# Optimization experiments

Measured on AMD Instinct MI355X. Metric: run time of the kernel, lower is better.

Reference implementation:

```python
import jax, jax.numpy as jnp
import numpy as np

N_USERS = 100000
N_ITEMS = 50000
N_NODES = N_USERS + N_ITEMS
DIM = 64
N_HOPS = 3
NNZ = 3200000
BATCH = 4096
K = 4
DECAY = 1e-4


def setup_inputs() -> dict:
    key = jax.random.key(0)
    ks = jax.random.split(key, 8)
    user_embed = jax.random.normal(ks[0], (N_USERS, DIM), dtype=jnp.float32) * 0.1
    item_embed = jax.random.normal(ks[1], (N_ITEMS, DIM), dtype=jnp.float32) * 0.1
    adj_rows = jax.random.randint(ks[2], (NNZ,), 0, N_NODES, dtype=jnp.int32)
    adj_cols = jax.random.randint(ks[3], (NNZ,), 0, N_NODES, dtype=jnp.int32)
    # normalized-adjacency-like small positive values
    adj_vals = jax.random.uniform(ks[4], (NNZ,), dtype=jnp.float32) * 0.05
    users = jax.random.randint(ks[5], (BATCH,), 0, N_USERS, dtype=jnp.int32)
    pos_items = jax.random.randint(ks[6], (BATCH,), 0, N_ITEMS, dtype=jnp.int32)
    neg_items = jax.random.randint(ks[7], (BATCH, K), 0, N_ITEMS, dtype=jnp.int32)
    return {"user_embed": user_embed, "item_embed": item_embed,
            "adj_vals": adj_vals, "adj_rows": adj_rows, "adj_cols": adj_cols,
            "users": users, "pos_items": pos_items, "neg_items": neg_items}


def _gcn(user_embed, item_embed, adj_vals, adj_rows, adj_cols):
    """LightGCN propagation: n_hops of SpMM, stack per-hop embeddings."""
    all_embed = jnp.concatenate([user_embed, item_embed], axis=0)  # [N, d]
    agg = all_embed
    embs = [all_embed]
    for _ in range(N_HOPS):
        msg = adj_vals[:, None] * agg[adj_cols]                    # [nnz, d]
        agg = jax.ops.segment_sum(msg, adj_rows, num_segments=N_NODES)
        embs.append(agg)
    embs = jnp.stack(embs, axis=1)                                 # [N, hops+1, d]
    return embs[:N_USERS], embs[N_USERS:]


def reference(user_embed, item_embed, adj_vals, adj_rows, adj_cols,
              users, pos_items, neg_items):
    user_gcn, item_gcn = _gcn(user_embed, item_embed, adj_vals, adj_rows, adj_cols)
    u_g = user_gcn[users]            # [B, hops+1, d]
    p_g = item_gcn[pos_items]        # [B, hops+1, d]
    n_g = item_gcn[neg_items]        # [B, K, hops+1, d]
    # pooling == 'mean' over hop axis
    u_e = u_g.mean(axis=1)
    pos_e = p_g.mean(axis=1)
    neg_e = n_g.mean(axis=2)         # [B, K, d]
    pos_scores = jnp.sum(u_e * pos_e, axis=-1)                     # [B]
    neg_scores = jnp.sum(u_e[:, None, :] * neg_e, axis=-1)         # [B, K]
    # BCE with logits: labels 1 for pos, 0 for neg
    pos_loss = jax.nn.softplus(-pos_scores)
    neg_loss = jax.nn.softplus(neg_scores).sum(axis=1)
    mf_loss = pos_loss + neg_loss
    regularize = (jnp.sum(u_g[:, 0, :] ** 2)
                  + jnp.sum(p_g[:, 0, :] ** 2)
                  + jnp.sum(n_g[:, :, 0, :] ** 2)) / 2.0
    emb_loss = DECAY * regularize / BATCH
    return mf_loss.mean() + emb_loss
```

## Files before the change

### kernel.cpp

```cpp
#include <hip/hip_runtime.h>
#include <hip/hip_bf16.h>
#include <math.h>

#define N_USERS 100000
#define N_ITEMS 50000
#define N_NODES 150000
#define DIM     64
#define N_HOPS  3
#define NNZ     3200000
#define BATCH   4096
#define KNEG    4
#define DECAY   1e-4f
#define BATCH_TOT (BATCH * (2 + KNEG))

#define NBUCK   586
#define NCHUNK  1024
#define CHUNK   (NNZ / NCHUNK)
#define CAP     8192
#define BH_N    (NBUCK * NCHUNK)
#define S1_N    ((BH_N + 255) / 256)
#define S2_N    ((S1_N + 255) / 256)

typedef unsigned short ushort_t;
typedef unsigned int uint_t;
typedef unsigned long long u64_t;
typedef float v2f __attribute__((ext_vector_type(2)));

#if __has_builtin(__builtin_amdgcn_cvt_pk_f32_fp8) && __has_builtin(__builtin_amdgcn_cvt_pk_fp8_f32)
#define HAVE_FP8_CVT 1
#else
#define HAVE_FP8_CVT 0
#endif

#if !HAVE_FP8_CVT
__device__ __forceinline__ float dec1_(uint_t b) {
    uint_t s = b >> 7, e = (b >> 3) & 15, m = b & 7;
    float mag = e ? __uint_as_float(((e + 120u) << 23) | (m << 20))
                  : (float)m * 0.001953125f;
    return s ? -mag : mag;
}
__device__ __forceinline__ uint_t enc1_(float x) {
    float ax = fabsf(x);
    uint_t s = (__float_as_uint(x) >> 31) << 7;
    if (!(ax > 0.f)) return s;
    if (ax >= 448.f) return s | 0x7E;
    if (ax < 0.015625f) {
        int m = (int)rintf(ax * 512.0f);
        if (m >= 8) return s | 0x08;
        return s | (uint_t)m;
    }
    uint_t u = __float_as_uint(ax);
    u += 0x7FFFF + ((u >> 20) & 1);
    int e = (int)((u >> 23) & 0xFF) - 127 + 7;
    if (e >= 16) return s | 0x7E;
    if (e <= 0)  return s | 0x08;
    return s | ((uint_t)e << 3) | ((u >> 20) & 7);
}
#endif

__device__ __forceinline__ void dec4(uint_t u, float* f) {
#if HAVE_FP8_CVT
    v2f lo = __builtin_amdgcn_cvt_pk_f32_fp8(u, false);
    v2f hi = __builtin_amdgcn_cvt_pk_f32_fp8(u, true);
    f[0] = lo[0]; f[1] = lo[1]; f[2] = hi[0]; f[3] = hi[1];
#else
    f[0] = dec1_(u & 255); f[1] = dec1_((u >> 8) & 255);
    f[2] = dec1_((u >> 16) & 255); f[3] = dec1_(u >> 24);
#endif
}

__device__ __forceinline__ uint_t enc4(const float* f) {
#if HAVE_FP8_CVT
    int t = __builtin_amdgcn_cvt_pk_fp8_f32(f[0], f[1], 0, false);
    t = __builtin_amdgcn_cvt_pk_fp8_f32(f[2], f[3], t, true);
    return (uint_t)t;
#else
    return enc1_(f[0]) | (enc1_(f[1]) << 8) | (enc1_(f[2]) << 16) | (enc1_(f[3]) << 24);
#endif
}


__global__ void k_bhist(const int* __restrict__ rows, int* __restrict__ bh) {
    __shared__ int hist[NBUCK];
    int t = threadIdx.x, b = blockIdx.x;
    for (int i = t; i < NBUCK; i += 256) hist[i] = 0;
    __syncthreads();
    int base = b * CHUNK;
    for (int e = base + t; e < base + CHUNK; e += 256)
        atomicAdd(&hist[rows[e] >> 8], 1);
    __syncthreads();
    for (int i = t; i < NBUCK; i += 256)
        bh[(size_t)i * NCHUNK + b] = hist[i];
}

__global__ void k_scanA(int* __restrict__ data, int* __restrict__ bsums, int n) {
    __shared__ int lds[256];
    int t = threadIdx.x;
    int i = blockIdx.x * 256 + t;
    int v = (i < n) ? data[i] : 0;
    lds[t] = v; __syncthreads();
    for (int o = 1; o < 256; o <<= 1) {
        int x = (t >= o) ? lds[t - o] : 0;
        __syncthreads();
        lds[t] += x;
        __syncthreads();
    }
    if (i < n) data[i] = lds[t] - v;
    if (t == 255) bsums[blockIdx.x] = lds[t];
}

__global__ void k_scan_small(int* __restrict__ data, int n) {
    __shared__ int lds[1024];
    int t = threadIdx.x;
    int v = (t < n) ? data[t] : 0;
    lds[t] = v; __syncthreads();
    for (int o = 1; o < 1024; o <<= 1) {
        int x = (t >= o) ? lds[t - o] : 0;
        __syncthreads();
        lds[t] += x;
        __syncthreads();
    }
    if (t < n) data[t] = lds[t] - v;
}

__global__ void k_addback(int* __restrict__ data, const int* __restrict__ offs, int n) {
    int i = blockIdx.x * blockDim.x + threadIdx.x;
    if (i < n) data[i] += offs[i >> 8];
}

__global__ void k_scatter(const int* __restrict__ rows, const int* __restrict__ cols,
                          const float* __restrict__ vals, const int* __restrict__ bh,
                          u64_t* __restrict__ ebuf) {
    __shared__ int offs[NBUCK];
    int t = threadIdx.x, b = blockIdx.x;
    for (int i = t; i < NBUCK; i += 256)
        offs[i] = bh[(size_t)i * NCHUNK + b];
    __syncthreads();
    int base = b * CHUNK;
    for (int e = base + t; e < base + CHUNK; e += 256) {
        int r = rows[e];
        int slot = atomicAdd(&offs[r >> 8], 1);
        u64_t pk = ((u64_t)(uint_t)__float_as_int(vals[e]) << 32)
                 | ((u64_t)(r & 255) << 18) | (u64_t)cols[e];
        ebuf[slot] = pk;
    }
}

__global__ void k_bucket_csr(const u64_t* __restrict__ ebuf, const int* __restrict__ bh,
                             int2* __restrict__ edges, int* __restrict__ row_ptr) {
    __shared__ u64_t stage[CAP];
    __shared__ int hist[256];
    __shared__ int sbuf[256];
    int t = threadIdx.x, b = blockIdx.x;
    int S = bh[(size_t)b * NCHUNK];
    int E = (b + 1 < NBUCK) ? bh[(size_t)(b + 1) * NCHUNK] : NNZ;
    int cnt = E - S;
    if (cnt > CAP) cnt = CAP;
    hist[t] = 0;
    __syncthreads();
    for (int i = t; i < cnt; i += 256) {
        u64_t v = ebuf[S + i];
        stage[i] = v;
        atomicAdd(&hist[(int)((v >> 18) & 255)], 1);
    }
    __syncthreads();
    int v = hist[t];
    sbuf[t] = v; __syncthreads();
    for (int o = 1; o < 256; o <<= 1) {
        int x = (t >= o) ? sbuf[t - o] : 0;
        __syncthreads();
        sbuf[t] += x;
        __syncthreads();
    }
    int excl = sbuf[t] - v;
    int grow = (b << 8) + t;
    if (grow < N_NODES) row_ptr[grow] = S + excl;
    if (b == 0 && t == 0) row_ptr[N_NODES] = NNZ;
    hist[t] = excl;
    __syncthreads();
    for (int i = t; i < cnt; i += 256) {
        u64_t pk = stage[i];
        int rl = (int)((pk >> 18) & 255);
        int slot = atomicAdd(&hist[rl], 1);
        edges[S + slot] = make_int2((int)(pk & 0x3FFFF), (int)(pk >> 32));
    }
}


__global__ void k_tofp8(const float* __restrict__ ue, const float* __restrict__ ie,
                        uint2* __restrict__ outq) {
    int idx = blockIdx.x * blockDim.x + threadIdx.x;
    const int total8 = N_NODES * DIM / 8;
    if (idx >= total8) return;
    const int u8 = N_USERS * DIM / 8;
    const float4* src = (idx < u8) ? (const float4*)ue + 2 * (size_t)idx
                                   : (const float4*)ie + 2 * (size_t)(idx - u8);
    float4 a = src[0], b = src[1];
    float fa[4] = {a.x, a.y, a.z, a.w};
    float fb[4] = {b.x, b.y, b.z, b.w};
    outq[idx] = make_uint2(enc4(fa), enc4(fb));
}

__device__ __forceinline__ void fma8(uint2 r, float v, float* acc) {
    float f[4];
    dec4(r.x, f);
    acc[0] += v * f[0]; acc[1] += v * f[1]; acc[2] += v * f[2]; acc[3] += v * f[3];
    dec4(r.y, f);
    acc[4] += v * f[0]; acc[5] += v * f[1]; acc[6] += v * f[2]; acc[7] += v * f[3];
}

__device__ __forceinline__ void row_accum8(const uint2* __restrict__ srcq,
                                           const int2* __restrict__ edges,
                                           int s, int e, int oct, int ol,
                                           float* acc) {
    int i = s;
    for (; i + 16 <= e; i += 16) {
        int2 e0 = edges[i + oct];
        int2 e1 = edges[i + 8 + oct];
        uint2 r0 = srcq[(size_t)e0.x * 8 + ol];
        uint2 r1 = srcq[(size_t)e1.x * 8 + ol];
        fma8(r0, __int_as_float(e0.y), acc);
        fma8(r1, __int_as_float(e1.y), acc);
    }
    for (; i + 8 <= e; i += 8) {
        int2 ed = edges[i + oct];
        uint2 r = srcq[(size_t)ed.x * 8 + ol];
        fma8(r, __int_as_float(ed.y), acc);
    }
    int rem = e - i;
    if (oct < rem) {
        int2 ed = edges[i + oct];
        uint2 r = srcq[(size_t)ed.x * 8 + ol];
        fma8(r, __int_as_float(ed.y), acc);
    }
}

__device__ __forceinline__ void oct_reduce(float* acc) {
    #pragma unroll
    for (int j = 0; j < 8; ++j) {
        acc[j] += __shfl_xor(acc[j], 8);
        acc[j] += __shfl_xor(acc[j], 16);
        acc[j] += __shfl_xor(acc[j], 32);
    }
}

__global__ void k_spmm(const uint2* __restrict__ srcq, uint2* __restrict__ outq,
                       const int* __restrict__ row_ptr, const int2* __restrict__ edges) {
    int w = (blockIdx.x * blockDim.x + threadIdx.x) >> 6;
    int lane = threadIdx.x & 63;
    if (w >= N_NODES) return;
    int oct = lane >> 3, ol = lane & 7;
    int s = row_ptr[w], e = row_ptr[w + 1];
    float acc[8] = {0.f, 0.f, 0.f, 0.f, 0.f, 0.f, 0.f, 0.f};
    row_accum8(srcq, edges, s, e, oct, ol, acc);
    oct_reduce(acc);
    if (oct == 0)
        outq[(size_t)w * 8 + ol] = make_uint2(enc4(acc), enc4(acc + 4));
}

__device__ __forceinline__ void batch_map(int w, const int* __restrict__ users,
                                          const int* __restrict__ pos, const int* __restrict__ neg,
                                          float* u_acc, float* p_acc, float* n_acc,
                                          int& node, float*& dst) {
    if (w < BATCH)            { node = users[w];                        dst = u_acc + (size_t)w * DIM; }
    else if (w < 2 * BATCH)   { int j = w - BATCH;     node = N_USERS + pos[j]; dst = p_acc + (size_t)j * DIM; }
    else                      { int j = w - 2 * BATCH; node = N_USERS + neg[j]; dst = n_acc + (size_t)j * DIM; }
}

__global__ void k_gather_init(const float* __restrict__ ue, const float* __restrict__ ie,
                              const int* __restrict__ users, const int* __restrict__ pos,
                              const int* __restrict__ neg,
                              float* __restrict__ u_acc, float* __restrict__ p_acc,
                              float* __restrict__ n_acc) {
    int w = (blockIdx.x * blockDim.x + threadIdx.x) >> 6;
    int lane = threadIdx.x & 63;
    if (w >= BATCH_TOT) return;
    int node; float* dst;
    batch_map(w, users, pos, neg, u_acc, p_acc, n_acc, node, dst);
    const float* srow = (node < N_USERS) ? ue + (size_t)node * DIM
                                         : ie + (size_t)(node - N_USERS) * DIM;
    dst[lane] = srow[lane];
}

__global__ void k_gather_accum(const uint_t* __restrict__ src,
                               const int* __restrict__ users, const int* __restrict__ pos,
                               const int* __restrict__ neg,
                               float* __restrict__ u_acc, float* __restrict__ p_acc,
                               float* __restrict__ n_acc) {
    int gid = blockIdx.x * blockDim.x + threadIdx.x;
    int w4 = gid >> 6;
    int lane = threadIdx.x & 63;
    int slot = w4 * 4 + (lane >> 4);
    int dquad = lane & 15;
    if (slot >= BATCH_TOT) return;
    int node; float* dst;
    batch_map(slot, users, pos, neg, u_acc, p_acc, n_acc, node, dst);
    float f[4];
    dec4(src[(size_t)node * 16 + dquad], f);
    float4* d4 = (float4*)(dst + 4 * dquad);
    float4 cur = *d4;
    cur.x += f[0]; cur.y += f[1]; cur.z += f[2]; cur.w += f[3];
    *d4 = cur;
}

__global__ void k_spmm_batch(const uint2* __restrict__ srcq,
                             const int* __restrict__ row_ptr, const int2* __restrict__ edges,
                             const int* __restrict__ users, const int* __restrict__ pos,
                             const int* __restrict__ neg,
                             float* __restrict__ u_acc, float* __restrict__ p_acc,
                             float* __restrict__ n_acc) {
    int w = (blockIdx.x * blockDim.x + threadIdx.x) >> 6;
    int lane = threadIdx.x & 63;
    if (w >= BATCH_TOT) return;
    int oct = lane >> 3, ol = lane & 7;
    int node; float* dst;
    batch_map(w, users, pos, neg, u_acc, p_acc, n_acc, node, dst);
    int s = row_ptr[node], e = row_ptr[node + 1];
    float acc[8] = {0.f, 0.f, 0.f, 0.f, 0.f, 0.f, 0.f, 0.f};
    row_accum8(srcq, edges, s, e, oct, ol, acc);
    oct_reduce(acc);
    if (oct == 0) {
        #pragma unroll
        for (int j = 0; j < 8; ++j) dst[8 * ol + j] += acc[j];
    }
}

__global__ void k_zero_out(float* out) { out[0] = 0.f; }

__device__ __forceinline__ float softplus(float x) {
    return log1pf(expf(-fabsf(x))) + fmaxf(x, 0.f);
}

__device__ __forceinline__ float wave_sum(float v) {
    for (int o = 32; o > 0; o >>= 1) v += __shfl_xor(v, o);
    return v;
}

__global__ void k_loss(const float* __restrict__ u_acc, const float* __restrict__ p_acc,
                       const float* __restrict__ n_acc,
                       const float* __restrict__ ue, const float* __restrict__ ie,
                       const int* __restrict__ users, const int* __restrict__ pos,
                       const int* __restrict__ neg, float* __restrict__ out) {
    int w = (blockIdx.x * blockDim.x + threadIdx.x) >> 6;
    int lane = threadIdx.x & 63;
    if (w >= BATCH) return;
    const float inv = 1.0f / (N_HOPS + 1);
    float u = u_acc[(size_t)w * DIM + lane] * inv;
    float p = p_acc[(size_t)w * DIM + lane] * inv;
    float pos_score = wave_sum(u * p);
    float loss = softplus(-pos_score);
    #pragma unroll
    for (int k = 0; k < KNEG; ++k) {
        float nk = n_acc[((size_t)w * KNEG + k) * DIM + lane] * inv;
        float neg_score = wave_sum(u * nk);
        loss += softplus(neg_score);
    }
    float u0 = ue[(size_t)users[w] * DIM + lane];
    float p0 = ie[(size_t)pos[w]  * DIM + lane];
    float r = u0 * u0 + p0 * p0;
    #pragma unroll
    for (int k = 0; k < KNEG; ++k) {
        float n0 = ie[(size_t)neg[w * KNEG + k] * DIM + lane];
        r += n0 * n0;
    }
    r = wave_sum(r);
    float contrib = loss * (1.0f / BATCH) + (DECAY * 0.5f / BATCH) * r;
    if (lane == 0) atomicAdd(out, contrib);
}


extern "C" void kernel_launch(void* const* d_in, const int* in_sizes, int n_in,
                              void* d_out, int out_size, void* d_ws, size_t ws_size,
                              hipStream_t stream) {
    const float* user_embed = (const float*)d_in[0];
    const float* item_embed = (const float*)d_in[1];
    const float* adj_vals   = (const float*)d_in[2];
    const int*   adj_rows   = (const int*)d_in[3];
    const int*   adj_cols   = (const int*)d_in[4];
    const int*   users      = (const int*)d_in[5];
    const int*   pos_items  = (const int*)d_in[6];
    const int*   neg_items  = (const int*)d_in[7];
    float* out = (float*)d_out;

    int2* edges   = (int2*)d_ws;
    u64_t* ebuf   = (u64_t*)(edges + NNZ);
    float* u_acc  = (float*)(ebuf + NNZ);
    float* p_acc  = u_acc + (size_t)BATCH * DIM;
    float* n_acc  = p_acc + (size_t)BATCH * DIM;
    uint2* bufB   = (uint2*)(n_acc + (size_t)BATCH * KNEG * DIM);
    uint2* buf1   = bufB + (size_t)N_NODES * 8;
    int* row_ptr  = (int*)(buf1 + (size_t)N_NODES * 8);
    int* bh       = row_ptr + N_NODES + 1;
    int* S1       = bh + BH_N;
    int* S2       = S1 + S1_N;
    uint2* buf0   = (uint2*)ebuf;

    const int T = 256;

    k_bhist<<<NCHUNK, 256, 0, stream>>>(adj_rows, bh);
    k_scanA<<<S1_N, 256, 0, stream>>>(bh, S1, BH_N);
    k_scanA<<<S2_N, 256, 0, stream>>>(S1, S2, S1_N);
    k_scan_small<<<1, 1024, 0, stream>>>(S2, S2_N);
    k_addback<<<(S1_N + T - 1) / T, T, 0, stream>>>(S1, S2, S1_N);
    k_addback<<<(BH_N + T - 1) / T, T, 0, stream>>>(bh, S1, BH_N);
    k_scatter<<<NCHUNK, 256, 0, stream>>>(adj_rows, adj_cols, adj_vals, bh, ebuf);
    k_bucket_csr<<<NBUCK, 256, 0, stream>>>(ebuf, bh, edges, row_ptr);

    k_tofp8<<<(N_NODES * DIM / 8 + T - 1) / T, T, 0, stream>>>(user_embed, item_embed, bufB);

    int gb = (BATCH_TOT * 64 + T - 1) / T;
    k_gather_init<<<gb, T, 0, stream>>>(user_embed, item_embed,
                                        users, pos_items, neg_items,
                                        u_acc, p_acc, n_acc);

    int sb = (N_NODES * 64 + T - 1) / T;
    int gb4 = ((BATCH_TOT / 4) * 64 + T - 1) / T;

    k_spmm<<<sb, T, 0, stream>>>(bufB, buf0, row_ptr, edges);
    k_gather_accum<<<gb4, T, 0, stream>>>((const uint_t*)buf0, users, pos_items, neg_items,
                                          u_acc, p_acc, n_acc);
    k_spmm<<<sb, T, 0, stream>>>(buf0, buf1, row_ptr, edges);
    k_gather_accum<<<gb4, T, 0, stream>>>((const uint_t*)buf1, users, pos_items, neg_items,
                                          u_acc, p_acc, n_acc);
    k_spmm_batch<<<gb, T, 0, stream>>>(buf1, row_ptr, edges,
                                       users, pos_items, neg_items,
                                       u_acc, p_acc, n_acc);

    k_zero_out<<<1, 1, 0, stream>>>(out);
    k_loss<<<(BATCH * 64 + T - 1) / T, T, 0, stream>>>(
        u_acc, p_acc, n_acc, user_embed, item_embed, users, pos_items, neg_items, out);
}
```

Before: 318.3 us.

## Stage edge scatter in LDS with local counting sort before bucket writes

The edge scatter kernel now counts bucket occupancy per chunk, prefix-sums it in shared memory, and places packed edges into an LDS staging array in bucket order. Each wavefront then copies contiguous per-bucket runs to the global edge buffer. This replaces scattered 8-byte global stores with short contiguous runs. Chunk count is halved and block size doubled so each chunk fits the shared-memory stage. The cost is a second read of the row indices, extra barriers, and a large LDS footprint per block that limits how many blocks can be resident at once.

```diff
diff --git a/kernel.cpp b/kernel.cpp
--- a/kernel.cpp
+++ b/kernel.cpp
@@ -14,7 +14,7 @@
 #define BATCH_TOT (BATCH * (2 + KNEG))
 
 #define NBUCK   586
-#define NCHUNK  1024
+#define NCHUNK  512
 #define CHUNK   (NNZ / NCHUNK)
 #define CAP     8192
 #define BH_N    (NBUCK * NCHUNK)
@@ -128,21 +128,54 @@
     if (i < n) data[i] += offs[i >> 8];
 }
 
-__global__ void k_scatter(const int* __restrict__ rows, const int* __restrict__ cols,
-                          const float* __restrict__ vals, const int* __restrict__ bh,
-                          u64_t* __restrict__ ebuf) {
-    __shared__ int offs[NBUCK];
+__global__ __launch_bounds__(512) void k_scatter(
+        const int* __restrict__ rows, const int* __restrict__ cols,
+        const float* __restrict__ vals, const int* __restrict__ bh,
+        u64_t* __restrict__ ebuf) {
+    __shared__ u64_t stage[CHUNK];
+    __shared__ int sexcl[NBUCK + 1];
+    __shared__ int gbase[NBUCK];
+    __shared__ int cursor[NBUCK];
+    __shared__ int part[512];
     int t = threadIdx.x, b = blockIdx.x;
-    for (int i = t; i < NBUCK; i += 256)
-        offs[i] = bh[(size_t)i * NCHUNK + b];
-    __syncthreads();
-    int base = b * CHUNK;
-    for (int e = base + t; e < base + CHUNK; e += 256) {
+    for (int i = t; i < NBUCK; i += 512) {
+        cursor[i] = 0;
+        gbase[i] = bh[(size_t)i * NCHUNK + b];
+    }
+    __syncthreads();
+    int base0 = b * CHUNK;
+    for (int e = base0 + t; e < base0 + CHUNK; e += 512)
+        atomicAdd(&cursor[rows[e] >> 8], 1);
+    __syncthreads();
+    int a0 = (2 * t     < NBUCK) ? cursor[2 * t]     : 0;
+    int a1 = (2 * t + 1 < NBUCK) ? cursor[2 * t + 1] : 0;
+    part[t] = a0 + a1;
+    __syncthreads();
+    for (int o = 1; o < 512; o <<= 1) {
+        int x = (t >= o) ? part[t - o] : 0;
+        __syncthreads();
+        part[t] += x;
+        __syncthreads();
+    }
+    int ebase = part[t] - (a0 + a1);
+    if (2 * t < NBUCK)     sexcl[2 * t] = ebase;
+    if (2 * t + 1 < NBUCK) sexcl[2 * t + 1] = ebase + a0;
+    if (t == 0) sexcl[NBUCK] = CHUNK;
+    __syncthreads();
+    for (int i = t; i < NBUCK; i += 512) cursor[i] = sexcl[i];
+    __syncthreads();
+    for (int e = base0 + t; e < base0 + CHUNK; e += 512) {
         int r = rows[e];
-        int slot = atomicAdd(&offs[r >> 8], 1);
-        u64_t pk = ((u64_t)(uint_t)__float_as_int(vals[e]) << 32)
-                 | ((u64_t)(r & 255) << 18) | (u64_t)cols[e];
-        ebuf[slot] = pk;
+        int slot = atomicAdd(&cursor[r >> 8], 1);
+        stage[slot] = ((u64_t)(uint_t)__float_as_int(vals[e]) << 32)
+                    | ((u64_t)(r & 255) << 18) | (u64_t)cols[e];
+    }
+    __syncthreads();
+    int wid = t >> 6, lane = t & 63;
+    for (int k = wid; k < NBUCK; k += 8) {
+        int S = sexcl[k], E = sexcl[k + 1], G = gbase[k];
+        for (int j = S + lane; j < E; j += 64)
+            ebuf[G + j - S] = stage[j];
     }
 }
 
@@ -403,7 +436,7 @@
     k_scan_small<<<1, 1024, 0, stream>>>(S2, S2_N);
     k_addback<<<(S1_N + T - 1) / T, T, 0, stream>>>(S1, S2, S1_N);
     k_addback<<<(BH_N + T - 1) / T, T, 0, stream>>>(bh, S1, BH_N);
-    k_scatter<<<NCHUNK, 256, 0, stream>>>(adj_rows, adj_cols, adj_vals, bh, ebuf);
+    k_scatter<<<NCHUNK, 512, 0, stream>>>(adj_rows, adj_cols, adj_vals, bh, ebuf);
     k_bucket_csr<<<NBUCK, 256, 0, stream>>>(ebuf, bh, edges, row_ptr);
 
     k_tofp8<<<(N_NODES * DIM / 8 + T - 1) / T, T, 0, stream>>>(user_embed, item_embed, bufB);
```

New measurement: 301.4 us. 1.06x faster.
